# Performance work log

Hardware: AMD Instinct MI355X
Metric: run time of the kernel (lower is better)

## Reference

```python
import jax, jax.numpy as jnp
import numpy as np

B, L, D = 2, 2048, 1024
H, QK, V = 8, 128, 128
EPS = 1e-5  # torch GroupNorm default


def setup_inputs() -> dict:
    key = jax.random.key(0)
    ks = jax.random.split(key, 6)
    sequence = jax.random.normal(ks[0], (B, L, D), jnp.float32)
    times = jnp.broadcast_to(jnp.arange(L, dtype=jnp.float32), (B, L))
    shift = D ** -0.5
    scale = 2.0 * shift
    w_q = jax.random.uniform(ks[1], (H, D, QK), jnp.float32) * scale - shift
    w_k = jax.random.uniform(ks[2], (H, D, QK), jnp.float32) * scale - shift
    w_v = jax.random.uniform(ks[3], (H, D, V), jnp.float32) * scale - shift
    out_dims = H * V
    w_g = jax.random.uniform(ks[4], (D, out_dims), jnp.float32) * scale - shift
    shift2 = out_dims ** -0.5
    scale2 = 2.0 * shift2
    w_o = jax.random.uniform(ks[5], (out_dims, out_dims), jnp.float32) * scale2 - shift2
    gn_w = jnp.ones((out_dims,), jnp.float32)
    gn_b = jnp.zeros((out_dims,), jnp.float32)
    return dict(sequence=sequence, times=times, w_q=w_q, w_k=w_k, w_v=w_v,
                w_g=w_g, w_o=w_o, gn_w=gn_w, gn_b=gn_b)


def rotate_by_i(x):
    # pairs (even, odd) -> (-odd, even), interleaved back
    x2 = x.reshape(x.shape[:-1] + (-1, 2))
    real, imag = x2[..., 0], x2[..., 1]
    return jnp.stack([-imag, real], axis=-1).reshape(x.shape)


def reference(sequence, times, w_q, w_k, w_v, w_g, w_o, gn_w, gn_b):
    gammas = 1.0 - 2.0 ** (-5.0 - jnp.arange(H, dtype=jnp.float32))            # (H,)
    thetas = 10000.0 ** (-2.0 * jnp.arange(QK // 2, dtype=jnp.float32) / QK)   # (QK/2,)

    q = jnp.einsum('bld,hdk->hblk', sequence, w_q)  # (H,B,L,QK)
    k = jnp.einsum('bld,hdk->hblk', sequence, w_k)
    v = jnp.einsum('bld,hdv->hblv', sequence, w_v)  # (H,B,L,V)

    # xPos rotor: angles interleaved-duplicated along last dim
    angles = times[..., None] * thetas              # (B,L,QK/2)
    cos = jnp.repeat(jnp.cos(angles), 2, axis=-1)   # (B,L,QK)
    sin = jnp.repeat(jnp.sin(angles), 2, axis=-1)
    q = cos * q + sin * rotate_by_i(q)
    k = cos * k - sin * rotate_by_i(k)

    # causal exponential-decay mask D[n,m] = gamma**(n-m) * (n>=m)
    mat = times[:, :, None] - times[:, None, :]     # (B,L,L)
    mask = mat >= 0
    g4 = gammas[:, None, None, None]                # (H,1,1,1)
    d = jnp.where(mask, g4 ** jnp.where(mask, mat, 0.0), 0.0)  # (H,B,L,L)

    ret = jnp.einsum('hbik,hbjk->hbij', q, k) * d   # (H,B,L,L)
    retention = jnp.einsum('hbij,hbjv->hbiv', ret, v)  # (H,B,L,V)

    # GroupNorm(num_heads, H*V): normalize each head's V channels per token
    r = jnp.transpose(retention, (1, 2, 0, 3))      # (B,L,H,V)
    mean = r.mean(-1, keepdims=True)
    var = r.var(-1, keepdims=True)
    rn = (r - mean) / jnp.sqrt(var + EPS)
    rn = rn * gn_w.reshape(H, V) + gn_b.reshape(H, V)
    rn = rn.reshape(B, L, H * V)

    g = sequence @ w_g
    gate = g * jax.nn.sigmoid(g)                    # swish
    return (gate * rn) @ w_o                        # (B,L,H*V)
```

## Files before the change

### kernel.cpp

```cpp
#include <hip/hip_runtime.h>
#include <stdint.h>

typedef unsigned short u16;
typedef unsigned int   u32;
typedef short  short8 __attribute__((ext_vector_type(8)));
typedef float  f32x4  __attribute__((ext_vector_type(4)));

#define DEV static __device__ __forceinline__

DEV float bf2f(u16 u) { u32 x = ((u32)u) << 16; float f; __builtin_memcpy(&f, &x, 4); return f; }
DEV u16 f2bf(float f) {
  u32 u; __builtin_memcpy(&u, &f, 4);
  return (u16)((u + 0x7FFFu + ((u >> 16) & 1u)) >> 16);
}
DEV bool probe_bf16(const void* times) { return *(const u32*)times == 0x3F800000u; }

DEV void gload16(const u16* g, u16* l) {
  __builtin_amdgcn_global_load_lds(
      (__attribute__((address_space(1))) void*)(u16*)g,
      (__attribute__((address_space(3))) void*)l, 16, 0, 0);
}

DEV f32x4 MFMA(short8 a, short8 b, f32x4 c) {
  return __builtin_amdgcn_mfma_f32_16x16x32_bf16(a, b, c, 0, 0, 0);
}

DEV void gemm128(const u16* Ag, const u16* Bg, int K, u16* sA, u16* sB,
                 f32x4 (&acc)[4][4]) {
  const int tid = threadIdx.x;
  const int lane = tid & 63, w = tid >> 6;
  const int wm = w >> 1, wn = w & 1;
  const int row = lane & 15, quad = lane >> 4;
  f32x4 z = {0.f, 0.f, 0.f, 0.f};
#pragma unroll
  for (int mt = 0; mt < 4; ++mt)
#pragma unroll
    for (int nt = 0; nt < 4; ++nt) acc[mt][nt] = z;

  for (int k0 = 0; k0 < K; k0 += 64) {
    __syncthreads();
#pragma unroll
    for (int i = 0; i < 4; ++i) {
      int c = (w << 2) + i;
      gload16(Ag + (size_t)(c * 8 + (lane >> 3)) * K + k0 + (lane & 7) * 8, sA + c * 544);
      gload16(Bg + (size_t)(c * 8 + (lane >> 3)) * K + k0 + (lane & 7) * 8, sB + c * 544);
    }
    __syncthreads();
#pragma unroll
    for (int kt = 0; kt < 2; ++kt) {
      short8 av[4], bv[4];
#pragma unroll
      for (int t = 0; t < 4; ++t) {
        int m = wm * 64 + t * 16 + row;
        av[t] = *(const short8*)(sA + (m >> 3) * 544 + (m & 7) * 64 + kt * 32 + quad * 8);
        int n = wn * 64 + t * 16 + row;
        bv[t] = *(const short8*)(sB + (n >> 3) * 544 + (n & 7) * 64 + kt * 32 + quad * 8);
      }
#pragma unroll
      for (int mt = 0; mt < 4; ++mt)
#pragma unroll
        for (int nt = 0; nt < 4; ++nt)
          acc[mt][nt] = MFMA(av[mt], bv[nt], acc[mt][nt]);
    }
  }
}

__global__ __launch_bounds__(256) void transpose_kernel(
    const void* wq, const void* wk, const void* wv, const void* wg,
    const void* wo, const void* times, u16* wsT) {
  __shared__ u16 T[128 * 132];
  int s = blockIdx.x, t = blockIdx.y;
  bool isbf = probe_bf16(times);
  const void* src; int ld; size_t off0;
  if (s < 8)       { src = wq; ld = 128;  off0 = (size_t)s * 131072; }
  else if (s < 16) { src = wk; ld = 128;  off0 = (size_t)(s - 8) * 131072; }
  else if (s < 24) { src = wv; ld = 128;  off0 = (size_t)(s - 16) * 131072; }
  else if (s < 32) { src = wg; ld = 1024; off0 = (size_t)(s - 24) * 128; }
  else             { src = wo; ld = 1024; off0 = (size_t)(s - 32) * 128; }
  int d0 = t * 128;
  const u16* s16 = (const u16*)src;
  const float* s32 = (const float*)src;
  for (int pass = 0; pass < 64; ++pass) {
    int idx = pass * 256 + threadIdx.x;
    int dl = idx >> 7, c = idx & 127;
    size_t goff = off0 + (size_t)(d0 + dl) * ld + c;
    T[c * 132 + dl] = isbf ? s16[goff] : f2bf(s32[goff]);
  }
  __syncthreads();
  u16* dst = wsT + (size_t)s * 131072;
  for (int pass = 0; pass < 16; ++pass) {
    int idx = pass * 256 + threadIdx.x;
    int c = idx >> 5, ch = idx & 31;
    uint2 v = *(const uint2*)&T[c * 132 + ch * 4];
    *(uint2*)&dst[(size_t)c * 1024 + d0 + ch * 4] = v;
  }
}

__global__ __launch_bounds__(256) void seq_kernel(const void* seq, const void* times, u16* dst) {
  bool isbf = probe_bf16(times);
  size_t idx = ((size_t)blockIdx.x * 256 + threadIdx.x) * 8;
  if (isbf) {
    *(uint4*)&dst[idx] = *(const uint4*)((const u16*)seq + idx);
  } else {
    const float* s = (const float*)seq;
    u32 a0 = (u32)f2bf(s[idx + 0]) | ((u32)f2bf(s[idx + 1]) << 16);
    u32 a1 = (u32)f2bf(s[idx + 2]) | ((u32)f2bf(s[idx + 3]) << 16);
    u32 a2 = (u32)f2bf(s[idx + 4]) | ((u32)f2bf(s[idx + 5]) << 16);
    u32 a3 = (u32)f2bf(s[idx + 6]) | ((u32)f2bf(s[idx + 7]) << 16);
    uint4 v; v.x = a0; v.y = a1; v.z = a2; v.w = a3;
    *(uint4*)&dst[idx] = v;
  }
}

__global__ __launch_bounds__(256, 2) void proj_kernel(
    const u16* seqb, const void* times, const u16* wsT,
    u16* qws, u16* kws, u16* vtws, u16* gatews) {
  __shared__ __align__(16) u16 smem[17408];
  u16* sA = smem;
  u16* sB = smem + 8704;
  int nb = blockIdx.x, mb = blockIdx.y;
  f32x4 acc[4][4];
  gemm128(seqb + (size_t)mb * 128 * 1024, wsT + (size_t)nb * 131072, 1024, sA, sB, acc);

  const int tid = threadIdx.x, lane = tid & 63, w = tid >> 6;
  const int wm = w >> 1, wn = w & 1, row = lane & 15, quad = lane >> 4;
  const bool isbf = probe_bf16(times);
  const u16* t16 = (const u16*)times;
  const float* t32 = (const float*)times;
  const int b = mb >> 4, l0 = (mb & 15) * 128;

  __syncthreads();

  if (nb < 16) {
    int type = nb >> 3;
    int h = nb & 7;
    float sgnk = type ? -1.f : 1.f;
#pragma unroll
    for (int mt = 0; mt < 4; ++mt) {
#pragma unroll
      for (int nt = 0; nt < 4; ++nt) {
        int c = wn * 64 + nt * 16 + row;
        float theta = exp2f(-0.2076205059304601f * (float)(c >> 1));
        float sgn = (c & 1) ? 1.f : -1.f;
#pragma unroll
        for (int r = 0; r < 4; ++r) {
          int lloc = wm * 64 + mt * 16 + quad * 4 + r;
          float v = acc[mt][nt][r];
          float pv = __shfl_xor(v, 1);
          float tv = isbf ? bf2f(t16[b * 2048 + l0 + lloc]) : t32[b * 2048 + l0 + lloc];
          float rev = theta * tv * 0.15915494309189535f;
          rev -= floorf(rev);
          float sn = __builtin_amdgcn_sinf(rev);
          float cs = __builtin_amdgcn_cosf(rev);
          float ov = cs * v + sgnk * sgn * sn * pv;
          u16 o16 = f2bf(ov);
          int other = __shfl_xor((int)o16, 1);
          if (!(lane & 1))
            *(u32*)&smem[lloc * 136 + c] = (u32)o16 | ((u32)other << 16);
        }
      }
    }
    __syncthreads();
    u16* outp = (type ? kws : qws) + (((size_t)(h * 2 + b) * 2048 + l0) << 7);
#pragma unroll
    for (int p = 0; p < 8; ++p) {
      int idx = p * 256 + tid, rr = idx >> 4, ch = idx & 15;
      *(uint4*)&outp[(size_t)rr * 128 + ch * 8] = *(const uint4*)&smem[rr * 136 + ch * 8];
    }
  } else if (nb < 24) {
    int h = nb & 7;
#pragma unroll
    for (int mt = 0; mt < 4; ++mt) {
      int lb = wm * 64 + mt * 16 + quad * 4;
#pragma unroll
      for (int nt = 0; nt < 4; ++nt) {
        int c = wn * 64 + nt * 16 + row;
        uint2 pk;
        pk.x = (u32)f2bf(acc[mt][nt][0]) | ((u32)f2bf(acc[mt][nt][1]) << 16);
        pk.y = (u32)f2bf(acc[mt][nt][2]) | ((u32)f2bf(acc[mt][nt][3]) << 16);
        *(uint2*)&smem[c * 136 + lb] = pk;
      }
    }
    __syncthreads();
    u16* outp = vtws + (size_t)(h * 2 + b) * 262144 + l0;
#pragma unroll
    for (int p = 0; p < 8; ++p) {
      int idx = p * 256 + tid, cc = idx >> 4, ch = idx & 15;
      *(uint4*)&outp[(size_t)cc * 2048 + ch * 8] = *(const uint4*)&smem[cc * 136 + ch * 8];
    }
  } else {
    int cb = nb - 24;
#pragma unroll
    for (int mt = 0; mt < 4; ++mt) {
#pragma unroll
      for (int nt = 0; nt < 4; ++nt) {
        int c = wn * 64 + nt * 16 + row;
#pragma unroll
        for (int r = 0; r < 4; ++r) {
          int lloc = wm * 64 + mt * 16 + quad * 4 + r;
          float x = acc[mt][nt][r];
          float s = x / (1.f + __expf(-x));
          u16 o16 = f2bf(s);
          int other = __shfl_xor((int)o16, 1);
          if (!(lane & 1))
            *(u32*)&smem[lloc * 136 + c] = (u32)o16 | ((u32)other << 16);
        }
      }
    }
    __syncthreads();
    u16* outp = gatews + (size_t)(mb * 128) * 1024 + (size_t)cb * 128;
#pragma unroll
    for (int p = 0; p < 8; ++p) {
      int idx = p * 256 + tid, rr = idx >> 4, ch = idx & 15;
      *(uint4*)&outp[(size_t)rr * 1024 + ch * 8] = *(const uint4*)&smem[rr * 136 + ch * 8];
    }
  }
}

__global__ __launch_bounds__(256, 1) void retention_kernel(
    const u16* qws, const u16* kws, const u16* vtws, const void* times, float* rws) {
  __shared__ __align__(16) u16 sK[32 * 528];
  __shared__ __align__(16) u16 sV[32 * 528];
  __shared__ __align__(16) u16 sP[128 * 136];
  const int ib = blockIdx.x, hb = blockIdx.y;
  const int h = hb >> 1, b = hb & 1;
  const int i0 = ib * 128;
  const int tid = threadIdx.x, lane = tid & 63, w = tid >> 6;
  const int wm = w >> 1, wn = w & 1, row = lane & 15, quad = lane >> 4;
  const bool isbf = probe_bf16(times);
  const u16* t16 = (const u16*)times;
  const float* t32 = (const float*)times;
  const float gamma = 1.f - exp2f(-5.f - (float)h);
  const float l2g = log2f(gamma);

  short8 qf[4][4];
  const u16* qbase = qws + ((size_t)hb * 2048 + i0) * 128;
#pragma unroll
  for (int mt = 0; mt < 4; ++mt)
#pragma unroll
    for (int kt = 0; kt < 4; ++kt)
      qf[mt][kt] = *(const short8*)(qbase + (size_t)(wm * 64 + mt * 16 + row) * 128 + kt * 32 + quad * 8);

  float trow[4][4], rpow[4][4];
#pragma unroll
  for (int mt = 0; mt < 4; ++mt)
#pragma unroll
    for (int r = 0; r < 4; ++r) {
      int i = i0 + wm * 64 + mt * 16 + quad * 4 + r;
      float tv = isbf ? bf2f(t16[b * 2048 + i]) : t32[b * 2048 + i];
      trow[mt][r] = tv;
      rpow[mt][r] = exp2f(l2g * (tv - (float)i0));
    }

  f32x4 z = {0.f, 0.f, 0.f, 0.f};
  f32x4 oacc[4][4];
#pragma unroll
  for (int mt = 0; mt < 4; ++mt)
#pragma unroll
    for (int nt = 0; nt < 4; ++nt) oacc[mt][nt] = z;

  const u16* kbase = kws + (size_t)hb * 262144;
  const u16* vbase = vtws + (size_t)hb * 262144;

  for (int jb = 0; jb <= ib; ++jb) {
    const int j0 = jb * 128;
    if (l2g * (float)(i0 - j0 - 258) < -57.f) continue;
    __syncthreads();
#pragma unroll
    for (int ii = 0; ii < 8; ++ii) {
      int c = w * 8 + ii;
      gload16(kbase + (size_t)(j0 + c * 4 + (lane >> 4)) * 128 + (lane & 15) * 8, sK + c * 528);
      gload16(vbase + (size_t)(c * 4 + (lane >> 4)) * 2048 + j0 + (lane & 15) * 8, sV + c * 528);
    }
    __syncthreads();

    f32x4 p[4][4];
#pragma unroll
    for (int mt = 0; mt < 4; ++mt)
#pragma unroll
      for (int nt = 0; nt < 4; ++nt) p[mt][nt] = z;
#pragma unroll
    for (int kt = 0; kt < 4; ++kt) {
      short8 bv[4];
#pragma unroll
      for (int nt = 0; nt < 4; ++nt) {
        int jr = wn * 64 + nt * 16 + row;
        bv[nt] = *(const short8*)(sK + (jr >> 2) * 528 + (jr & 3) * 128 + kt * 32 + quad * 8);
      }
#pragma unroll
      for (int mt = 0; mt < 4; ++mt)
#pragma unroll
        for (int nt = 0; nt < 4; ++nt)
          p[mt][nt] = MFMA(qf[mt][kt], bv[nt], p[mt][nt]);
    }

    float tcol[4], cp[4];
#pragma unroll
    for (int nt = 0; nt < 4; ++nt) {
      int j = j0 + wn * 64 + nt * 16 + row;
      float tv = isbf ? bf2f(t16[b * 2048 + j]) : t32[b * 2048 + j];
      tcol[nt] = tv;
      cp[nt] = exp2f(l2g * ((float)i0 - tv));
    }
    bool intra = (jb == ib);
#pragma unroll
    for (int mt = 0; mt < 4; ++mt)
#pragma unroll
      for (int nt = 0; nt < 4; ++nt)
#pragma unroll
        for (int r = 0; r < 4; ++r) {
          float f = rpow[mt][r] * cp[nt];
          float val = p[mt][nt][r] * f;
          if (intra && (trow[mt][r] < tcol[nt])) val = 0.f;
          sP[(wm * 64 + mt * 16 + quad * 4 + r) * 136 + wn * 64 + nt * 16 + row] = f2bf(val);
        }
    __syncthreads();

#pragma unroll
    for (int kt = 0; kt < 4; ++kt) {
      short8 av[4], bv[4];
#pragma unroll
      for (int mt = 0; mt < 4; ++mt)
        av[mt] = *(const short8*)(sP + (wm * 64 + mt * 16 + row) * 136 + kt * 32 + quad * 8);
#pragma unroll
      for (int nt = 0; nt < 4; ++nt) {
        int v = wn * 64 + nt * 16 + row;
        bv[nt] = *(const short8*)(sV + (v >> 2) * 528 + (v & 3) * 128 + kt * 32 + quad * 8);
      }
#pragma unroll
      for (int mt = 0; mt < 4; ++mt)
#pragma unroll
        for (int nt = 0; nt < 4; ++nt)
          oacc[mt][nt] = MFMA(av[mt], bv[nt], oacc[mt][nt]);
    }
  }

#pragma unroll
  for (int mt = 0; mt < 4; ++mt)
#pragma unroll
    for (int nt = 0; nt < 4; ++nt)
#pragma unroll
      for (int r = 0; r < 4; ++r) {
        int i = i0 + wm * 64 + mt * 16 + quad * 4 + r;
        int v = wn * 64 + nt * 16 + row;
        rws[((size_t)hb * 2048 + i) * 128 + v] = oacc[mt][nt][r];
      }
}

__global__ __launch_bounds__(256) void norm_kernel(
    const float* rws, const u16* gatews, const void* gnw, const void* gnb,
    const void* times, u16* xws) {
  int tid = threadIdx.x, lane = tid & 63, w = tid >> 6;
  int rid = blockIdx.x * 4 + w;
  int hb = rid >> 11, l = rid & 2047, h = hb >> 1, b = hb & 1;
  bool isbf = probe_bf16(times);
  float2 xv = *(const float2*)&rws[(size_t)rid * 128 + lane * 2];
  float s = xv.x + xv.y, ss = xv.x * xv.x + xv.y * xv.y;
#pragma unroll
  for (int o = 1; o < 64; o <<= 1) { s += __shfl_xor(s, o); ss += __shfl_xor(ss, o); }
  float mean = s * (1.f / 128.f);
  float var = fmaxf(ss * (1.f / 128.f) - mean * mean, 0.f);
  float inv = rsqrtf(var + 1e-5f);
  int c0 = h * 128 + lane * 2;
  float g0, g1, bb0, bb1;
  if (isbf) {
    g0 = bf2f(((const u16*)gnw)[c0]); g1 = bf2f(((const u16*)gnw)[c0 + 1]);
    bb0 = bf2f(((const u16*)gnb)[c0]); bb1 = bf2f(((const u16*)gnb)[c0 + 1]);
  } else {
    g0 = ((const float*)gnw)[c0]; g1 = ((const float*)gnw)[c0 + 1];
    bb0 = ((const float*)gnb)[c0]; bb1 = ((const float*)gnb)[c0 + 1];
  }
  float y0 = (xv.x - mean) * inv * g0 + bb0;
  float y1 = (xv.y - mean) * inv * g1 + bb1;
  size_t xi = ((size_t)(b * 2048 + l)) * 1024 + c0;
  float gt0 = bf2f(gatews[xi]), gt1 = bf2f(gatews[xi + 1]);
  u32 pk = (u32)f2bf(y0 * gt0) | ((u32)f2bf(y1 * gt1) << 16);
  *(u32*)&xws[xi] = pk;
}

__global__ __launch_bounds__(256, 2) void out_kernel(
    const u16* xws, const u16* wsT, const void* times, void* dout) {
  __shared__ __align__(16) u16 smem[17408];
  u16* sA = smem;
  u16* sB = smem + 8704;
  int nb = blockIdx.x, mb = blockIdx.y;
  f32x4 acc[4][4];
  gemm128(xws + (size_t)mb * 128 * 1024, wsT + (size_t)(32 + nb) * 131072, 1024, sA, sB, acc);
  const int tid = threadIdx.x, lane = tid & 63, w = tid >> 6;
  const int wm = w >> 1, wn = w & 1, row = lane & 15, quad = lane >> 4;
  bool isbf = probe_bf16(times);
  if (isbf) {
    __syncthreads();
#pragma unroll
    for (int mt = 0; mt < 4; ++mt) {
#pragma unroll
      for (int nt = 0; nt < 4; ++nt) {
        int c = wn * 64 + nt * 16 + row;
#pragma unroll
        for (int r = 0; r < 4; ++r) {
          int lloc = wm * 64 + mt * 16 + quad * 4 + r;
          u16 o16 = f2bf(acc[mt][nt][r]);
          int other = __shfl_xor((int)o16, 1);
          if (!(lane & 1))
            *(u32*)&smem[lloc * 136 + c] = (u32)o16 | ((u32)other << 16);
        }
      }
    }
    __syncthreads();
    u16* outp = (u16*)dout + (size_t)(mb * 128) * 1024 + (size_t)nb * 128;
#pragma unroll
    for (int p = 0; p < 8; ++p) {
      int idx = p * 256 + tid, rr = idx >> 4, ch = idx & 15;
      *(uint4*)&outp[(size_t)rr * 1024 + ch * 8] = *(const uint4*)&smem[rr * 136 + ch * 8];
    }
  } else {
#pragma unroll
    for (int mt = 0; mt < 4; ++mt)
#pragma unroll
      for (int nt = 0; nt < 4; ++nt)
#pragma unroll
        for (int r = 0; r < 4; ++r) {
          int i = mb * 128 + wm * 64 + mt * 16 + quad * 4 + r;
          size_t o = (size_t)i * 1024 + nb * 128 + wn * 64 + nt * 16 + row;
          ((float*)dout)[o] = acc[mt][nt][r];
        }
  }
}

extern "C" void kernel_launch(void* const* d_in, const int* in_sizes, int n_in,
                              void* d_out, int out_size, void* d_ws, size_t ws_size,
                              hipStream_t stream) {
  const void* seq   = d_in[0];
  const void* times = d_in[1];
  const void* wq = d_in[2];
  const void* wk = d_in[3];
  const void* wv = d_in[4];
  const void* wg = d_in[5];
  const void* wo = d_in[6];
  const void* gnw = d_in[7];
  const void* gnb = d_in[8];

  u16* ws = (u16*)d_ws;
  u16* wsT    = ws;
  u16* qws    = ws + 5242880;
  u16* kws    = qws + 4194304;
  u16* vtws   = kws + 4194304;
  u16* gatews = vtws + 4194304;
  float* rws  = (float*)(gatews + 4194304);
  u16* seqb   = (u16*)(rws + 4194304);
  u16* xws    = qws;

  transpose_kernel<<<dim3(40, 8), 256, 0, stream>>>(wq, wk, wv, wg, wo, times, wsT);
  seq_kernel<<<dim3(2048), 256, 0, stream>>>(seq, times, seqb);
  proj_kernel<<<dim3(32, 32), 256, 0, stream>>>(seqb, times, wsT, qws, kws, vtws, gatews);
  retention_kernel<<<dim3(16, 16), 256, 0, stream>>>(qws, kws, vtws, times, rws);
  norm_kernel<<<dim3(8192), 256, 0, stream>>>(rws, gatews, gnw, gnb, times, xws);
  out_kernel<<<dim3(8, 32), 256, 0, stream>>>(xws, wsT, times, d_out);
}
```

Before: 273.9 us.

## Split retention key blocks across workgroups with atomic accumulation and shared LDS

Result: slower. 318.4 us (+16.3%).

```diff
diff --git a/kernel.cpp b/kernel.cpp
--- a/kernel.cpp
+++ b/kernel.cpp
@@ -112,6 +112,12 @@
   }
 }
 
+__global__ __launch_bounds__(256) void zero_kernel(float* p) {
+  size_t i = ((size_t)blockIdx.x * 256 + threadIdx.x) * 4;
+  f32x4 z = {0.f, 0.f, 0.f, 0.f};
+  *(f32x4*)&p[i] = z;
+}
+
 __global__ __launch_bounds__(256, 2) void proj_kernel(
     const u16* seqb, const void* times, const u16* wsT,
     u16* qws, u16* kws, u16* vtws, u16* gatews) {
@@ -217,12 +223,22 @@
   }
 }
 
-__global__ __launch_bounds__(256, 1) void retention_kernel(
+__global__ __launch_bounds__(256, 2) void retention_kernel(
     const u16* qws, const u16* kws, const u16* vtws, const void* times, float* rws) {
-  __shared__ __align__(16) u16 sK[32 * 528];
-  __shared__ __align__(16) u16 sV[32 * 528];
-  __shared__ __align__(16) u16 sP[128 * 136];
-  const int ib = blockIdx.x, hb = blockIdx.y;
+  __shared__ __align__(16) u16 smem[17408 + 16896];
+  u16* sKP = smem;
+  u16* sV  = smem + 17408;
+
+  const int x = 39 - (int)blockIdx.x;
+  int ib, c0;
+  if (x < 4)       { ib = x;               c0 = 0; }
+  else if (x < 12) { int t = x - 4;  ib = 4 + (t >> 1); c0 = t & 1; }
+  else if (x < 24) { int t = x - 12; ib = 8 + t / 3;    c0 = t - (t / 3) * 3; }
+  else             { int t = x - 24; ib = 12 + (t >> 2); c0 = t & 3; }
+  const int jb_lo = c0 * 4;
+  const int jb_hi = min(jb_lo + 3, ib);
+
+  const int hb = blockIdx.y;
   const int h = hb >> 1, b = hb & 1;
   const int i0 = ib * 128;
   const int tid = threadIdx.x, lane = tid & 63, w = tid >> 6;
@@ -261,15 +277,17 @@
 
   const u16* kbase = kws + (size_t)hb * 262144;
   const u16* vbase = vtws + (size_t)hb * 262144;
-
-  for (int jb = 0; jb <= ib; ++jb) {
+  bool any = false;
+
+  for (int jb = jb_lo; jb <= jb_hi; ++jb) {
     const int j0 = jb * 128;
     if (l2g * (float)(i0 - j0 - 258) < -57.f) continue;
+    any = true;
     __syncthreads();
 #pragma unroll
     for (int ii = 0; ii < 8; ++ii) {
       int c = w * 8 + ii;
-      gload16(kbase + (size_t)(j0 + c * 4 + (lane >> 4)) * 128 + (lane & 15) * 8, sK + c * 528);
+      gload16(kbase + (size_t)(j0 + c * 4 + (lane >> 4)) * 128 + (lane & 15) * 8, sKP + c * 528);
       gload16(vbase + (size_t)(c * 4 + (lane >> 4)) * 2048 + j0 + (lane & 15) * 8, sV + c * 528);
     }
     __syncthreads();
@@ -285,7 +303,7 @@
 #pragma unroll
       for (int nt = 0; nt < 4; ++nt) {
         int jr = wn * 64 + nt * 16 + row;
-        bv[nt] = *(const short8*)(sK + (jr >> 2) * 528 + (jr & 3) * 128 + kt * 32 + quad * 8);
+        bv[nt] = *(const short8*)(sKP + (jr >> 2) * 528 + (jr & 3) * 128 + kt * 32 + quad * 8);
       }
 #pragma unroll
       for (int mt = 0; mt < 4; ++mt)
@@ -293,6 +311,7 @@
         for (int nt = 0; nt < 4; ++nt)
           p[mt][nt] = MFMA(qf[mt][kt], bv[nt], p[mt][nt]);
     }
+    __syncthreads();
 
     float tcol[4], cp[4];
 #pragma unroll
@@ -312,7 +331,7 @@
           float f = rpow[mt][r] * cp[nt];
           float val = p[mt][nt][r] * f;
           if (intra && (trow[mt][r] < tcol[nt])) val = 0.f;
-          sP[(wm * 64 + mt * 16 + quad * 4 + r) * 136 + wn * 64 + nt * 16 + row] = f2bf(val);
+          sKP[(wm * 64 + mt * 16 + quad * 4 + r) * 136 + wn * 64 + nt * 16 + row] = f2bf(val);
         }
     __syncthreads();
 
@@ -321,7 +340,7 @@
       short8 av[4], bv[4];
 #pragma unroll
       for (int mt = 0; mt < 4; ++mt)
-        av[mt] = *(const short8*)(sP + (wm * 64 + mt * 16 + row) * 136 + kt * 32 + quad * 8);
+        av[mt] = *(const short8*)(sKP + (wm * 64 + mt * 16 + row) * 136 + kt * 32 + quad * 8);
 #pragma unroll
       for (int nt = 0; nt < 4; ++nt) {
         int v = wn * 64 + nt * 16 + row;
@@ -335,16 +354,18 @@
     }
   }
 
-#pragma unroll
-  for (int mt = 0; mt < 4; ++mt)
-#pragma unroll
-    for (int nt = 0; nt < 4; ++nt)
-#pragma unroll
-      for (int r = 0; r < 4; ++r) {
-        int i = i0 + wm * 64 + mt * 16 + quad * 4 + r;
-        int v = wn * 64 + nt * 16 + row;
-        rws[((size_t)hb * 2048 + i) * 128 + v] = oacc[mt][nt][r];
-      }
+  if (any) {
+#pragma unroll
+    for (int mt = 0; mt < 4; ++mt)
+#pragma unroll
+      for (int nt = 0; nt < 4; ++nt)
+#pragma unroll
+        for (int r = 0; r < 4; ++r) {
+          int i = i0 + wm * 64 + mt * 16 + quad * 4 + r;
+          int v = wn * 64 + nt * 16 + row;
+          unsafeAtomicAdd(&rws[((size_t)hb * 2048 + i) * 128 + v], oacc[mt][nt][r]);
+        }
+  }
 }
 
 __global__ __launch_bounds__(256) void norm_kernel(
@@ -452,8 +473,9 @@
 
   transpose_kernel<<<dim3(40, 8), 256, 0, stream>>>(wq, wk, wv, wg, wo, times, wsT);
   seq_kernel<<<dim3(2048), 256, 0, stream>>>(seq, times, seqb);
+  zero_kernel<<<dim3(4096), 256, 0, stream>>>(rws);
   proj_kernel<<<dim3(32, 32), 256, 0, stream>>>(seqb, times, wsT, qws, kws, vtws, gatews);
-  retention_kernel<<<dim3(16, 16), 256, 0, stream>>>(qws, kws, vtws, times, rws);
+  retention_kernel<<<dim3(40, 16), 256, 0, stream>>>(qws, kws, vtws, times, rws);
   norm_kernel<<<dim3(8192), 256, 0, stream>>>(rws, gatews, gnw, gnb, times, xws);
   out_kernel<<<dim3(8, 32), 256, 0, stream>>>(xws, wsT, times, d_out);
 }
```
